# Kernel optimization log

Measured on AMD Instinct MI355X. Metric: run time of the kernel, lower is better.

Reference implementation:

```python
import jax, jax.numpy as jnp
import numpy as np

NV = 1_000_000   # number of 'var' nodes
NC = 500_000     # number of 'con' nodes
E = 16_000_000   # number of v2c edges (c2v is the reverse edge set)
H = 10           # n_h_feats


def setup_inputs() -> dict:
    key = jax.random.key(0)
    ks = jax.random.split(key, 24)
    s = 0.1  # weight init scale
    inp = {
        "var_c": jax.random.normal(ks[0], (NV,), jnp.float32),
        "var_x": jax.random.normal(ks[1], (NV,), jnp.float32),
        "con_b": jax.random.normal(ks[2], (NC,), jnp.float32),
        "A": jax.random.uniform(ks[3], (E,), jnp.float32),
        "src": jax.random.randint(ks[4], (E,), 0, NV, jnp.int32),
        "dst": jax.random.randint(ks[5], (E,), 0, NC, jnp.int32),
        # var_emb / con_emb Linear params
        "Wv": jax.random.normal(ks[6], (2, H), jnp.float32) * s,
        "bv": jnp.zeros((H,), jnp.float32),
        "Wc": jax.random.normal(ks[7], (1, H), jnp.float32) * s,
        "bc": jnp.zeros((H,), jnp.float32),
        # conv1 (GraphConv, shared across v2c/c2v) -- note: its output is
        # overwritten in the original forward and never reaches the output
        "W1": jax.random.normal(ks[8], (H, H), jnp.float32) * s,
        "b1": jnp.zeros((H,), jnp.float32),
        # conv2 (GraphConv, shared across v2c/c2v)
        "W2": jax.random.normal(ks[9], (H, H), jnp.float32) * s,
        "b2": jnp.zeros((H,), jnp.float32),
        # output MLP
        "Wo1": jax.random.normal(ks[10], (H, H), jnp.float32) * s,
        "bo1": jnp.zeros((H,), jnp.float32),
        "Wo2": jax.random.normal(ks[11], (H, H), jnp.float32) * s,
        "bo2": jnp.zeros((H,), jnp.float32),
        "Wo3": jax.random.normal(ks[12], (H, 1), jnp.float32) * s,
        "bo3": jnp.zeros((1,), jnp.float32),
    }
    return inp


def _gconv(x_src, W, b, s_idx, d_idx, ew, norm_src, norm_dst, n_dst):
    # DGL GraphConv, norm='both', with edge weights; in==out feats so W first.
    h = (x_src * norm_src) @ W                      # [N_src, H]
    msg = h[s_idx] * ew[:, None]                    # gather + edge weight
    agg = jax.ops.segment_sum(msg, d_idx, num_segments=n_dst)
    return agg * norm_dst + b


def reference(var_c, var_x, con_b, A, src, dst,
              Wv, bv, Wc, bc, W1, b1, W2, b2,
              Wo1, bo1, Wo2, bo2, Wo3, bo3):
    # symmetric norm from UNWEIGHTED degrees (DGL GraphConv norm='both'),
    # clamped at 1. v2c: out-deg(var), in-deg(con); c2v is the reverse.
    ones_e = jnp.ones_like(A)
    deg_v = jnp.clip(jax.ops.segment_sum(ones_e, src, num_segments=NV), 1.0)
    deg_c = jnp.clip(jax.ops.segment_sum(ones_e, dst, num_segments=NC), 1.0)
    norm_v = deg_v[:, None] ** -0.5
    norm_c = deg_c[:, None] ** -0.5

    # node embeddings
    var_feats = jnp.stack([var_c, var_x], axis=1)   # [NV, 2]
    X_var = jax.nn.relu(var_feats @ Wv + bv)        # [NV, H]
    X_con = jax.nn.relu(con_b[:, None] @ Wc + bc)   # [NC, H] (unused by convs: GraphConv ignores dst feats)

    # In the original forward, conv1 outputs (h_con / h_var) are immediately
    # overwritten by conv2 outputs (GraphConv only consumes src features),
    # so only conv2 lies on the effective compute path.
    h_con = jax.nn.relu(_gconv(X_var, W2, b2, src, dst, A, norm_v, norm_c, NC))
    h_var = jax.nn.relu(_gconv(h_con, W2, b2, dst, src, A, norm_c, norm_v, NV))

    h = jax.nn.relu(h_var @ Wo1 + bo1)
    h = jax.nn.relu(h @ Wo2 + bo2)
    logit = h @ Wo3 + bo3                           # [NV, 1]
    # dgl.readout_nodes(op='mean', ntype='var'), single graph -> [1, 1]
    return jnp.mean(logit, axis=0, keepdims=True)
```

## Files before the change

kernel.cpp:

```cpp
#include <hip/hip_runtime.h>

#define HF 10
#define ST 16
#define BST 16
#define SLC 256
#define NBINS 4096


__global__ __launch_bounds__(1024) void k_hist(const int* __restrict__ idx,
                                               unsigned* __restrict__ hist,
                                               long long s_begin, long long s_end, int per) {
    __shared__ unsigned l[NBINS];
    int t = threadIdx.x, sl = blockIdx.x;
    for (int b = t; b < NBINS; b += 1024) l[b] = 0u;
    __syncthreads();
    long long s0 = s_begin + (long long)sl * per;
    long long s1 = s0 + per; if (s1 > s_end) s1 = s_end;
    for (long long i = s0 + t; i < s1; i += 1024)
        atomicAdd(&l[((unsigned)idx[i]) >> 8], 1u);
    __syncthreads();
    unsigned* out = hist + (size_t)sl * NBINS;
    for (int b = t; b < NBINS; b += 1024) out[b] = l[b];
}

__global__ void k_coltot(const unsigned* __restrict__ h, unsigned* __restrict__ colT) {
    int b = blockIdx.x * 256 + threadIdx.x;
    unsigned s = 0u;
    for (int sl = 0; sl < SLC; sl++) s += h[(size_t)sl * NBINS + b];
    colT[b] = s;
}

__global__ __launch_bounds__(1024) void k_prefix(const unsigned* __restrict__ colT,
                                                 unsigned* __restrict__ start) {
    __shared__ unsigned p[1024];
    int t = threadIdx.x;
    uint4 v = *(const uint4*)(colT + 4 * t);
    unsigned own = v.x + v.y + v.z + v.w;
    p[t] = own;
    __syncthreads();
    for (int off = 1; off < 1024; off <<= 1) {
        unsigned u = (t >= off) ? p[t - off] : 0u;
        __syncthreads();
        p[t] += u;
        __syncthreads();
    }
    unsigned e = p[t] - own;
    *(uint4*)(start + 4 * t) = make_uint4(e, e + v.x, e + v.x + v.y, e + v.x + v.y + v.z);
    if (t == 1023) start[NBINS] = p[1023];
}

__global__ void k_offs(unsigned* __restrict__ h, const unsigned* __restrict__ start) {
    int b = blockIdx.x * 256 + threadIdx.x;
    unsigned cur = start[b];
    for (int sl = 0; sl < SLC; sl++) {
        unsigned* cell = h + (size_t)sl * NBINS + b;
        unsigned v = *cell;
        *cell = cur;
        cur += v;
    }
}

__global__ __launch_bounds__(1024) void k_scatS(const int* __restrict__ src, const int* __restrict__ dst,
                                                const float* __restrict__ A,
                                                const unsigned* __restrict__ offs,
                                                uint2* __restrict__ ebufS,
                                                long long E, int per) {
    __shared__ unsigned cur[NBINS];
    int t = threadIdx.x, sl = blockIdx.x;
    const unsigned* o = offs + (size_t)sl * NBINS;
    for (int b = t; b < NBINS; b += 1024) cur[b] = o[b];
    __syncthreads();
    long long s0 = (long long)sl * per;
    long long s1 = s0 + per; if (s1 > E) s1 = E;
    for (long long i = s0 + t; i < s1; i += 1024) {
        unsigned s = (unsigned)src[i], d = (unsigned)dst[i];
        float a = A[i];
        unsigned pos = atomicAdd(&cur[s >> 8], 1u);
        ebufS[pos] = make_uint2(((s & 255u) << 19) | d, __float_as_uint(a));
    }
}

__global__ void k_cntS2(const uint2* __restrict__ ebufS, const unsigned* __restrict__ startS,
                        const float* __restrict__ var_c, const float* __restrict__ var_x,
                        float4* __restrict__ vcx, int NV) {
    __shared__ unsigned cnt[256];
    int t = threadIdx.x, b = blockIdx.x;
    cnt[t] = 0u;
    __syncthreads();
    unsigned i0 = startS[b], i1 = startS[b + 1];
    for (unsigned i = i0 + t; i < i1; i += 256)
        atomicAdd(&cnt[ebufS[i].x >> 19], 1u);
    __syncthreads();
    int v = b * 256 + t;
    if (v < NV)
        vcx[v] = make_float4(var_c[v], var_x[v], rsqrtf(fmaxf((float)cnt[t], 1.0f)), 0.0f);
}

__global__ __launch_bounds__(1024) void k_scatD(const int* __restrict__ src, const int* __restrict__ dst,
                                                const float* __restrict__ A,
                                                const unsigned* __restrict__ offs,
                                                const float4* __restrict__ vcx,
                                                uint4* __restrict__ ebufD,
                                                long long s_begin, long long s_end, int per) {
    __shared__ unsigned cur[NBINS];
    int t = threadIdx.x, sl = blockIdx.x;
    const unsigned* o = offs + (size_t)sl * NBINS;
    for (int b = t; b < NBINS; b += 1024) cur[b] = o[b];
    __syncthreads();
    long long s0 = s_begin + (long long)sl * per;
    long long s1 = s0 + per; if (s1 > s_end) s1 = s_end;
    for (long long i = s0 + t; i < s1; i += 4096) {
        unsigned sv[4], dv[4]; float av[4]; bool hv[4];
#pragma unroll
        for (int j = 0; j < 4; j++) {
            long long idx = i + (long long)j * 1024;
            hv[j] = idx < s1;
            if (hv[j]) { sv[j] = (unsigned)src[idx]; dv[j] = (unsigned)dst[idx]; av[j] = A[idx]; }
            else       { sv[j] = 0u; dv[j] = 0u; av[j] = 0.0f; }
        }
        float4 g[4];
#pragma unroll
        for (int j = 0; j < 4; j++)
            if (hv[j]) g[j] = vcx[sv[j]];
#pragma unroll
        for (int j = 0; j < 4; j++) {
            if (!hv[j]) continue;
            unsigned pos = atomicAdd(&cur[dv[j] >> 8], 1u);
            ebufD[pos] = make_uint4(dv[j] & 255u, __float_as_uint(av[j] * g[j].z),
                                    __float_as_uint(g[j].x), __float_as_uint(g[j].y));
        }
    }
}

__global__ void k_aggD(const uint4* __restrict__ ebufD, const unsigned* __restrict__ startD,
                       const float* __restrict__ Wv, const float* __restrict__ bv,
                       float* __restrict__ bufC, float* __restrict__ deg_c, int NC) {
    __shared__ float acc[256 * HF];
    __shared__ unsigned cnt[256];
    int t = threadIdx.x, b = blockIdx.x;
    for (int i = t; i < 256 * HF; i += 256) acc[i] = 0.0f;
    cnt[t] = 0u;
    float wv0[HF], wv1[HF], bvv[HF];
#pragma unroll
    for (int h = 0; h < HF; h++) { wv0[h] = Wv[h]; wv1[h] = Wv[HF + h]; bvv[h] = bv[h]; }
    __syncthreads();
    unsigned i0 = startD[b], i1 = startD[b + 1];
    for (unsigned i = i0 + t; i < i1; i += 256) {
        uint4 kv = ebufD[i];
        unsigned dl = kv.x;
        float anv = __uint_as_float(kv.y);
        float c   = __uint_as_float(kv.z);
        float x   = __uint_as_float(kv.w);
        float* ac = acc + dl * HF;
#pragma unroll
        for (int h = 0; h < HF; h++) {
            float e = fmaxf(fmaf(c, wv0[h], fmaf(x, wv1[h], bvv[h])), 0.0f);
            atomicAdd(ac + h, anv * e);
        }
        atomicAdd(&cnt[dl], 1u);
    }
    __syncthreads();
    int gid = b * 256 + t;
    if (gid < NC) {
        float* row = bufC + (size_t)gid * BST;
#pragma unroll
        for (int h = 0; h < HF; h++) row[h] += acc[t * HF + h];
        deg_c[gid] += (float)cnt[t];
    }
}

__global__ void k_conT(float* __restrict__ bufC, const float* __restrict__ deg_c,
                       const float* __restrict__ W2, const float* __restrict__ b2, int NC) {
    __shared__ float sW[HF * HF], sb[HF];
    int t = threadIdx.x;
    if (t < HF * HF) sW[t] = W2[t];
    if (t < HF)      sb[t] = b2[t];
    __syncthreads();
    int i = blockIdx.x * 256 + t;
    if (i >= NC) return;
    float nc = rsqrtf(fmaxf(deg_c[i], 1.0f));
    float* row = bufC + (size_t)i * BST;
    float x[HF];
#pragma unroll
    for (int h = 0; h < HF; h++) x[h] = row[h];
#pragma unroll
    for (int j = 0; j < HF; j++) {
        float a = 0.0f;
#pragma unroll
        for (int k = 0; k < HF; k++) a = fmaf(x[k], sW[k * HF + j], a);
        row[j] = fmaxf(fmaf(a, nc, sb[j]), 0.0f) * nc;
    }
}

__global__ void k_aggS(const uint2* __restrict__ ebufS, const unsigned* __restrict__ startS,
                       const float* __restrict__ bufC, const float4* __restrict__ vcx,
                       const float* __restrict__ W2, const float* __restrict__ b2,
                       const float* __restrict__ Wo1, const float* __restrict__ bo1,
                       const float* __restrict__ Wo2, const float* __restrict__ bo2,
                       const float* __restrict__ Wo3, const float* __restrict__ bo3,
                       double* __restrict__ gacc, int NV) {
    __shared__ float acc[256 * HF];
    __shared__ float sW2[HF * HF], sb2[HF], sW1[HF * HF], sb1[HF], sWm[HF * HF], sbm[HF], sW3[HF];
    __shared__ float sb3;
    __shared__ double red[256];
    int t = threadIdx.x, b = blockIdx.x;
    for (int i = t; i < 256 * HF; i += 256) acc[i] = 0.0f;
    if (t < HF * HF) { sW2[t] = W2[t]; sW1[t] = Wo1[t]; sWm[t] = Wo2[t]; }
    if (t < HF)      { sb2[t] = b2[t]; sb1[t] = bo1[t]; sbm[t] = bo2[t]; sW3[t] = Wo3[t]; }
    if (t == 0)      sb3 = bo3[0];
    __syncthreads();
    unsigned i0 = startS[b], i1 = startS[b + 1];
    int grp = t >> 2;
    int q   = t & 3;
    int nq  = (q < 2) ? 4 : (q == 2 ? 2 : 0);
    for (unsigned base = i0; base < i1; base += 64) {
        unsigned e = base + (unsigned)grp;
        bool ok = e < i1;
        uint2 kv = ok ? ebufS[e] : make_uint2(0u, 0u);
        float4 y = make_float4(0.f, 0.f, 0.f, 0.f);
        if (ok) y = *(const float4*)(bufC + (size_t)(kv.x & 0x7FFFFu) * BST + 4 * q);
        if (ok && nq) {
            float a = __uint_as_float(kv.y);
            float* ac = acc + (kv.x >> 19) * HF + 4 * q;
            atomicAdd(ac + 0, a * y.x);
            atomicAdd(ac + 1, a * y.y);
            if (nq == 4) {
                atomicAdd(ac + 2, a * y.z);
                atomicAdd(ac + 3, a * y.w);
            }
        }
    }
    __syncthreads();
    double local = 0.0;
    int v = b * 256 + t;
    if (v < NV) {
        float nv = vcx[v].z;
        float x[HF], hvv[HF], h1[HF], h2[HF];
#pragma unroll
        for (int h = 0; h < HF; h++) x[h] = acc[t * HF + h];
#pragma unroll
        for (int j = 0; j < HF; j++) {
            float a = 0.0f;
#pragma unroll
            for (int k = 0; k < HF; k++) a = fmaf(x[k], sW2[k * HF + j], a);
            hvv[j] = fmaxf(fmaf(a, nv, sb2[j]), 0.0f);
        }
#pragma unroll
        for (int j = 0; j < HF; j++) {
            float a = sb1[j];
#pragma unroll
            for (int k = 0; k < HF; k++) a = fmaf(hvv[k], sW1[k * HF + j], a);
            h1[j] = fmaxf(a, 0.0f);
        }
#pragma unroll
        for (int j = 0; j < HF; j++) {
            float a = sbm[j];
#pragma unroll
            for (int k = 0; k < HF; k++) a = fmaf(h1[k], sWm[k * HF + j], a);
            h2[j] = fmaxf(a, 0.0f);
        }
        float logit = sb3;
#pragma unroll
        for (int k = 0; k < HF; k++) logit = fmaf(h2[k], sW3[k], logit);
        local = (double)logit;
    }
    red[t] = local;
    __syncthreads();
    for (int s = 128; s > 0; s >>= 1) {
        if (t < s) red[t] += red[t + s];
        __syncthreads();
    }
    if (t == 0) atomicAdd(gacc, red[0]);
}

__global__ void k_out(const double* __restrict__ acc, float* __restrict__ out, int NV) {
    out[0] = (float)(acc[0] / (double)NV);
}


__global__ void k_degree(const int* __restrict__ src, const int* __restrict__ dst,
                         float* __restrict__ deg_v, float* __restrict__ deg_c, int E) {
    int i = blockIdx.x * blockDim.x + threadIdx.x;
    if (i < E) {
        atomicAdd(&deg_v[src[i]], 1.0f);
        atomicAdd(&deg_c[dst[i]], 1.0f);
    }
}

__global__ void k_norm(float* __restrict__ d, int n) {
    int i = blockIdx.x * blockDim.x + threadIdx.x;
    if (i < n) d[i] = 1.0f / sqrtf(fmaxf(d[i], 1.0f));
}

__global__ void k_var_emb(const float* __restrict__ var_c, const float* __restrict__ var_x,
                          const float* __restrict__ norm_v,
                          const float* __restrict__ Wv, const float* __restrict__ bv,
                          const float* __restrict__ W2,
                          float* __restrict__ out, int NV) {
    __shared__ float sWv[2 * HF], sbv[HF], sW2[HF * HF];
    int t = threadIdx.x;
    if (t < 2 * HF) sWv[t] = Wv[t];
    if (t < HF)     sbv[t] = bv[t];
    if (t < HF * HF) sW2[t] = W2[t];
    __syncthreads();
    int i = blockIdx.x * blockDim.x + t;
    if (i >= NV) return;
    float c = var_c[i], x = var_x[i], nv = norm_v[i];
    float e[HF];
#pragma unroll
    for (int h = 0; h < HF; h++)
        e[h] = fmaxf(fmaf(c, sWv[h], fmaf(x, sWv[HF + h], sbv[h])), 0.0f) * nv;
    float* row = out + (size_t)i * ST;
#pragma unroll
    for (int j = 0; j < HF; j++) {
        float acc = 0.0f;
#pragma unroll
        for (int k = 0; k < HF; k++) acc = fmaf(e[k], sW2[k * HF + j], acc);
        row[j] = acc;
    }
}

__global__ void k_edge(const int* __restrict__ gidx, const int* __restrict__ didx,
                       const float* __restrict__ A,
                       const float* __restrict__ h, float* __restrict__ agg, int E) {
    int tid = blockIdx.x * blockDim.x + threadIdx.x;
    int e = tid / 5;
    if (e >= E) return;
    int q = tid - e * 5;
    int s = gidx[e], d = didx[e];
    float a = A[e];
    const float2 m = *(const float2*)(h + (size_t)s * ST + 2 * q);
    float* o = agg + (size_t)d * ST + 2 * q;
    atomicAdd(o,     m.x * a);
    atomicAdd(o + 1, m.y * a);
}

__global__ void k_con(float* __restrict__ buf, const float* __restrict__ norm_c,
                      const float* __restrict__ W2, const float* __restrict__ b2, int NC) {
    __shared__ float sW2[HF * HF], sb2[HF];
    int t = threadIdx.x;
    if (t < HF * HF) sW2[t] = W2[t];
    if (t < HF)      sb2[t] = b2[t];
    __syncthreads();
    int i = blockIdx.x * blockDim.x + t;
    if (i >= NC) return;
    float nc = norm_c[i];
    float* row = buf + (size_t)i * ST;
    float hc[HF];
#pragma unroll
    for (int h = 0; h < HF; h++)
        hc[h] = fmaxf(fmaf(row[h], nc, sb2[h]), 0.0f) * nc;
#pragma unroll
    for (int j = 0; j < HF; j++) {
        float acc = 0.0f;
#pragma unroll
        for (int k = 0; k < HF; k++) acc = fmaf(hc[k], sW2[k * HF + j], acc);
        row[j] = acc;
    }
}

__global__ void k_final(const float* __restrict__ agg_v, const float* __restrict__ norm_v,
                        const float* __restrict__ b2,
                        const float* __restrict__ Wo1, const float* __restrict__ bo1,
                        const float* __restrict__ Wo2, const float* __restrict__ bo2,
                        const float* __restrict__ Wo3, const float* __restrict__ bo3,
                        double* __restrict__ acc, int NV) {
    __shared__ float sb2[HF], sW1[HF * HF], sb1[HF], sW2m[HF * HF], sb2m[HF], sW3[HF];
    __shared__ float sb3;
    __shared__ double red[256];
    int t = threadIdx.x;
    if (t < HF)      sb2[t]  = b2[t];
    if (t < HF * HF) sW1[t]  = Wo1[t];
    if (t < HF)      sb1[t]  = bo1[t];
    if (t < HF * HF) sW2m[t] = Wo2[t];
    if (t < HF)      sb2m[t] = bo2[t];
    if (t < HF)      sW3[t]  = Wo3[t];
    if (t == 0)      sb3     = bo3[0];
    __syncthreads();
    int i = blockIdx.x * blockDim.x + t;
    double local = 0.0;
    if (i < NV) {
        float nv = norm_v[i];
        const float* row = agg_v + (size_t)i * ST;
        float v[HF], h1[HF], h2[HF];
#pragma unroll
        for (int h = 0; h < HF; h++) v[h] = fmaxf(fmaf(row[h], nv, sb2[h]), 0.0f);
#pragma unroll
        for (int j = 0; j < HF; j++) {
            float a = sb1[j];
#pragma unroll
            for (int k = 0; k < HF; k++) a = fmaf(v[k], sW1[k * HF + j], a);
            h1[j] = fmaxf(a, 0.0f);
        }
#pragma unroll
        for (int j = 0; j < HF; j++) {
            float a = sb2m[j];
#pragma unroll
            for (int k = 0; k < HF; k++) a = fmaf(h1[k], sW2m[k * HF + j], a);
            h2[j] = fmaxf(a, 0.0f);
        }
        float logit = sb3;
#pragma unroll
        for (int k = 0; k < HF; k++) logit = fmaf(h2[k], sW3[k], logit);
        local = (double)logit;
    }
    red[t] = local;
    __syncthreads();
    for (int s = 128; s > 0; s >>= 1) {
        if (t < s) red[t] += red[t + s];
        __syncthreads();
    }
    if (t == 0) atomicAdd(acc, red[0]);
}


extern "C" void kernel_launch(void* const* d_in, const int* in_sizes, int n_in,
                              void* d_out, int out_size, void* d_ws, size_t ws_size,
                              hipStream_t stream) {
    const float* var_c = (const float*)d_in[0];
    const float* var_x = (const float*)d_in[1];
    const float* A   = (const float*)d_in[3];
    const int*   src = (const int*)d_in[4];
    const int*   dst = (const int*)d_in[5];
    const float* Wv  = (const float*)d_in[6];
    const float* bv  = (const float*)d_in[7];
    const float* W2  = (const float*)d_in[12];
    const float* b2  = (const float*)d_in[13];
    const float* Wo1 = (const float*)d_in[14];
    const float* bo1 = (const float*)d_in[15];
    const float* Wo2 = (const float*)d_in[16];
    const float* bo2 = (const float*)d_in[17];
    const float* Wo3 = (const float*)d_in[18];
    const float* bo3 = (const float*)d_in[19];

    const int NV = in_sizes[0];
    const int NC = in_sizes[2];
    const int E  = in_sizes[3];

    auto layout_bytes = [&](int nDc, size_t* offs_out) -> size_t {
        size_t off = 0;
        auto alloc = [&](size_t bytes, int slot) {
            if (offs_out) offs_out[slot] = off;
            off = (off + bytes + 255) & ~(size_t)255;
        };
        size_t EcMax = ((size_t)E + nDc - 1) / nDc;
        alloc((size_t)NC * BST * 4, 0);
        alloc((size_t)NV * 16, 1);
        alloc((size_t)NC * 4, 2);
        alloc((size_t)SLC * NBINS * 4, 3);
        alloc((size_t)SLC * NBINS * 4, 4);
        alloc((size_t)NBINS * 4, 5);
        alloc((size_t)(NBINS + 1) * 4, 6);
        alloc((size_t)(NBINS + 1) * 4, 7);
        alloc(8, 8);
        alloc((size_t)E * 8, 9);
        alloc(EcMax * 16, 10);
        return off;
    };

    int nD = 0;
    size_t offs[11];
    for (int cand = 2; cand <= 16; cand++) {
        if (layout_bytes(cand, nullptr) <= ws_size) { nD = cand; break; }
    }
    bool fast = (nD > 0) && (NV <= (1 << 20)) && (NC <= (1 << 19)) && (E > 0);

    char* ws = (char*)d_ws;
    if (fast) {
        layout_bytes(nD, offs);
        float*    bufC   = (float*)(ws + offs[0]);
        float4*   vcx    = (float4*)(ws + offs[1]);
        float*    deg_c  = (float*)(ws + offs[2]);
        unsigned* hS     = (unsigned*)(ws + offs[3]);
        unsigned* hD     = (unsigned*)(ws + offs[4]);
        unsigned* colT   = (unsigned*)(ws + offs[5]);
        unsigned* startS = (unsigned*)(ws + offs[6]);
        unsigned* startD = (unsigned*)(ws + offs[7]);
        double*   gacc   = (double*)(ws + offs[8]);
        uint2*    ebufS  = (uint2*)(ws + offs[9]);
        uint4*    ebufD  = (uint4*)(ws + offs[10]);

        const long long EcMax = ((long long)E + nD - 1) / nD;
        const int perS = (int)(((long long)E + SLC - 1) / SLC);
        const int perD = (int)((EcMax + SLC - 1) / SLC);
        const int NB_S = (NV + 255) >> 8;
        const int NB_C = (NC + 255) >> 8;

        hipMemsetAsync(bufC,  0, (size_t)NC * BST * 4, stream);
        hipMemsetAsync(deg_c, 0, (size_t)NC * 4, stream);
        hipMemsetAsync(gacc,  0, 8, stream);

        k_hist<<<SLC, 1024, 0, stream>>>(src, hS, 0, E, perS);
        k_coltot<<<NBINS / 256, 256, 0, stream>>>(hS, colT);
        k_prefix<<<1, 1024, 0, stream>>>(colT, startS);
        k_offs<<<NBINS / 256, 256, 0, stream>>>(hS, startS);
        k_scatS<<<SLC, 1024, 0, stream>>>(src, dst, A, hS, ebufS, E, perS);

        k_cntS2<<<NB_S, 256, 0, stream>>>(ebufS, startS, var_c, var_x, vcx, NV);

        for (int c = 0; c < nD; c++) {
            long long cb = (long long)c * EcMax;
            long long ce = cb + EcMax; if (ce > E) ce = E;
            k_hist<<<SLC, 1024, 0, stream>>>(dst, hD, cb, ce, perD);
            k_coltot<<<NBINS / 256, 256, 0, stream>>>(hD, colT);
            k_prefix<<<1, 1024, 0, stream>>>(colT, startD);
            k_offs<<<NBINS / 256, 256, 0, stream>>>(hD, startD);
            k_scatD<<<SLC, 1024, 0, stream>>>(src, dst, A, hD, vcx, ebufD, cb, ce, perD);
            k_aggD<<<NB_C, 256, 0, stream>>>(ebufD, startD, Wv, bv, bufC, deg_c, NC);
        }
        k_conT<<<NB_C, 256, 0, stream>>>(bufC, deg_c, W2, b2, NC);

        k_aggS<<<NB_S, 256, 0, stream>>>(ebufS, startS, bufC, vcx, W2, b2,
                                         Wo1, bo1, Wo2, bo2, Wo3, bo3, gacc, NV);
        k_out<<<1, 1, 0, stream>>>(gacc, (float*)d_out, NV);
    } else {
        const int B = 256;
        float* fbufV = (float*)ws;
        float* fbufC = (float*)(ws + (size_t)NV * ST * 4);
        float* deg_v = (float*)(ws + (size_t)(NV + NC) * ST * 4);
        float* deg_c = deg_v + NV;
        size_t acc_off = ((size_t)(NV + NC) * ST * 4 + (size_t)(NV + NC) * 4 + 7) & ~(size_t)7;
        double* acc = (double*)(ws + acc_off);

        hipMemsetAsync(deg_v, 0, (size_t)(NV + NC) * 4, stream);
        hipMemsetAsync(fbufC, 0, (size_t)NC * ST * 4, stream);
        hipMemsetAsync(acc, 0, sizeof(double), stream);

        k_degree<<<(E + B - 1) / B, B, 0, stream>>>(src, dst, deg_v, deg_c, E);
        k_norm<<<(NV + NC + B - 1) / B, B, 0, stream>>>(deg_v, NV + NC);
        k_var_emb<<<(NV + B - 1) / B, B, 0, stream>>>(var_c, var_x, deg_v, Wv, bv, W2, fbufV, NV);

        long long tE = (long long)E * 5;
        k_edge<<<(int)((tE + B - 1) / B), B, 0, stream>>>(src, dst, A, fbufV, fbufC, E);
        k_con<<<(NC + B - 1) / B, B, 0, stream>>>(fbufC, deg_c, W2, b2, NC);

        hipMemsetAsync(fbufV, 0, (size_t)NV * ST * 4, stream);
        k_edge<<<(int)((tE + B - 1) / B), B, 0, stream>>>(dst, src, A, fbufC, fbufV, E);

        k_final<<<(NV + B - 1) / B, B, 0, stream>>>(fbufV, deg_v, b2, Wo1, bo1, Wo2, bo2, Wo3, bo3, acc, NV);
        k_out<<<1, 1, 0, stream>>>(acc, (float*)d_out, NV);
    }
}
```

Before: 3.009 ms.

## Sub-sort src-bucketed edges by dst slice and build dst chunks from them

Adds a second partitioning pass that splits each src bucket into 8 dst-slices (by the high bits of dst), so the edge buffer is ordered by src bin, then dst slice. The dst-side chunked histogram and scatter now read this pre-sorted buffer per src-bin range instead of re-reading the raw src/dst/A arrays. Each chunk then gathers vcx with locality (contiguous var bins) rather than randomly. The cost is two extra full passes over the edge buffer and a scratch buffer sized for the worst-case chunk, which relies on a heuristic bound that could overflow on skewed inputs.

```diff
diff --git a/kernel.cpp b/kernel.cpp
--- a/kernel.cpp
+++ b/kernel.cpp
@@ -5,6 +5,7 @@
 #define BST 16
 #define SLC 256
 #define NBINS 4096
+#define NSL 8
 
 
 __global__ __launch_bounds__(1024) void k_hist(const int* __restrict__ idx,
@@ -80,6 +81,36 @@
     }
 }
 
+__global__ void k_sliceCnt(const uint2* __restrict__ ebufA, const unsigned* __restrict__ startS,
+                           unsigned* __restrict__ startS2) {
+    __shared__ unsigned c8[NSL];
+    int t = threadIdx.x, b = blockIdx.x;
+    if (t < NSL) c8[t] = 0u;
+    __syncthreads();
+    unsigned i0 = startS[b], i1 = startS[b + 1];
+    for (unsigned i = i0 + t; i < i1; i += 256)
+        atomicAdd(&c8[(ebufA[i].x & 0x7FFFFu) >> 16], 1u);
+    __syncthreads();
+    if (t == 0) {
+        unsigned run = i0;
+        for (int s = 0; s < NSL; s++) { startS2[b * NSL + s] = run; run += c8[s]; }
+    }
+}
+
+__global__ void k_sliceScat(const uint2* __restrict__ ebufA, const unsigned* __restrict__ startS,
+                            const unsigned* __restrict__ startS2, uint2* __restrict__ ebufB) {
+    __shared__ unsigned cur[NSL];
+    int t = threadIdx.x, b = blockIdx.x;
+    if (t < NSL) cur[t] = startS2[b * NSL + t];
+    __syncthreads();
+    unsigned i0 = startS[b], i1 = startS[b + 1];
+    for (unsigned i = i0 + t; i < i1; i += 256) {
+        uint2 kv = ebufA[i];
+        unsigned pos = atomicAdd(&cur[(kv.x & 0x7FFFFu) >> 16], 1u);
+        ebufB[pos] = kv;
+    }
+}
+
 __global__ void k_cntS2(const uint2* __restrict__ ebufS, const unsigned* __restrict__ startS,
                         const float* __restrict__ var_c, const float* __restrict__ var_x,
                         float4* __restrict__ vcx, int NV) {
@@ -94,6 +125,48 @@
     int v = b * 256 + t;
     if (v < NV)
         vcx[v] = make_float4(var_c[v], var_x[v], rsqrtf(fmaxf((float)cnt[t], 1.0f)), 0.0f);
+}
+
+__global__ __launch_bounds__(1024) void k_histD2(const uint2* __restrict__ ebufB,
+                                                 const unsigned* __restrict__ startS,
+                                                 unsigned* __restrict__ hist, int B0, int binsPer) {
+    __shared__ unsigned l[NBINS];
+    int t = threadIdx.x, sl = blockIdx.x;
+    for (int b = t; b < NBINS; b += 1024) l[b] = 0u;
+    __syncthreads();
+    int b0 = B0 + sl * binsPer;
+    unsigned i0 = startS[b0], i1 = startS[b0 + binsPer];
+    for (unsigned i = i0 + t; i < i1; i += 1024)
+        atomicAdd(&l[(ebufB[i].x & 0x7FFFFu) >> 8], 1u);
+    __syncthreads();
+    unsigned* out = hist + (size_t)sl * NBINS;
+    for (int b = t; b < NBINS; b += 1024) out[b] = l[b];
+}
+
+__global__ __launch_bounds__(1024) void k_scatD2(const uint2* __restrict__ ebufB,
+                                                 const unsigned* __restrict__ startS,
+                                                 const unsigned* __restrict__ offs,
+                                                 const float4* __restrict__ vcx,
+                                                 uint4* __restrict__ ebufD, int B0, int binsPer) {
+    __shared__ unsigned cur[NBINS];
+    int t = threadIdx.x, sl = blockIdx.x;
+    const unsigned* o = offs + (size_t)sl * NBINS;
+    for (int b = t; b < NBINS; b += 1024) cur[b] = o[b];
+    __syncthreads();
+    int b0 = B0 + sl * binsPer;
+    for (int bb = 0; bb < binsPer; bb++) {
+        int bin = b0 + bb;
+        unsigned vbase = ((unsigned)bin) << 8;
+        unsigned i0 = startS[bin], i1 = startS[bin + 1];
+        for (unsigned i = i0 + t; i < i1; i += 1024) {
+            uint2 kv = ebufB[i];
+            unsigned d = kv.x & 0x7FFFFu;
+            float4 g = vcx[vbase | (kv.x >> 19)];
+            unsigned pos = atomicAdd(&cur[d >> 8], 1u);
+            ebufD[pos] = make_uint4(d & 255u, __float_as_uint(__uint_as_float(kv.y) * g.z),
+                                    __float_as_uint(g.x), __float_as_uint(g.y));
+        }
+    }
 }
 
 __global__ __launch_bounds__(1024) void k_scatD(const int* __restrict__ src, const int* __restrict__ dst,
@@ -437,13 +510,22 @@
     const int NC = in_sizes[2];
     const int E  = in_sizes[3];
 
-    auto layout_bytes = [&](int nDc, size_t* offs_out) -> size_t {
+    auto layout_bytes = [&](int nDc, bool split, size_t* offs_out) -> size_t {
         size_t off = 0;
         auto alloc = [&](size_t bytes, int slot) {
             if (offs_out) offs_out[slot] = off;
             off = (off + bytes + 255) & ~(size_t)255;
         };
-        size_t EcMax = ((size_t)E + nDc - 1) / nDc;
+        size_t EcMax;
+        if (split) {
+            long long vspan = (long long)(NBINS / nDc) * 256;
+            if (vspan > NV) vspan = NV;
+            long long ec = ((long long)E * vspan + NV - 1) / NV + (long long)E / 64;
+            if (ec > E) ec = E;
+            EcMax = (size_t)ec;
+        } else {
+            EcMax = ((size_t)E + nDc - 1) / nDc;
+        }
         alloc((size_t)NC * BST * 4, 0);
         alloc((size_t)NV * 16, 1);
         alloc((size_t)NC * 4, 2);
@@ -454,20 +536,28 @@
         alloc((size_t)(NBINS + 1) * 4, 7);
         alloc(8, 8);
         alloc((size_t)E * 8, 9);
-        alloc(EcMax * 16, 10);
+        size_t scratch = EcMax * 16;
+        if (split && scratch < (size_t)E * 8) scratch = (size_t)E * 8;
+        alloc(scratch, 10);
+        alloc(split ? (size_t)NBINS * NSL * 4 : (size_t)0, 11);
         return off;
     };
 
     int nD = 0;
-    size_t offs[11];
-    for (int cand = 2; cand <= 16; cand++) {
-        if (layout_bytes(cand, nullptr) <= ws_size) { nD = cand; break; }
+    bool split = false;
+    size_t offs[12];
+    for (int cand : {2, 4, 8, 16}) {
+        if (layout_bytes(cand, true, nullptr) <= ws_size) { nD = cand; split = true; break; }
+    }
+    if (nD == 0) {
+        for (int cand = 2; cand <= 16; cand++)
+            if (layout_bytes(cand, false, nullptr) <= ws_size) { nD = cand; break; }
     }
     bool fast = (nD > 0) && (NV <= (1 << 20)) && (NC <= (1 << 19)) && (E > 0);
 
     char* ws = (char*)d_ws;
     if (fast) {
-        layout_bytes(nD, offs);
+        layout_bytes(nD, split, offs);
         float*    bufC   = (float*)(ws + offs[0]);
         float4*   vcx    = (float4*)(ws + offs[1]);
         float*    deg_c  = (float*)(ws + offs[2]);
@@ -477,12 +567,11 @@
         unsigned* startS = (unsigned*)(ws + offs[6]);
         unsigned* startD = (unsigned*)(ws + offs[7]);
         double*   gacc   = (double*)(ws + offs[8]);
-        uint2*    ebufS  = (uint2*)(ws + offs[9]);
-        uint4*    ebufD  = (uint4*)(ws + offs[10]);
-
-        const long long EcMax = ((long long)E + nD - 1) / nD;
+        uint2*    ebufP  = (uint2*)(ws + offs[9]);
+        char*     scr    = ws + offs[10];
+        unsigned* startS2 = (unsigned*)(ws + offs[11]);
+
         const int perS = (int)(((long long)E + SLC - 1) / SLC);
-        const int perD = (int)((EcMax + SLC - 1) / SLC);
         const int NB_S = (NV + 255) >> 8;
         const int NB_C = (NC + 255) >> 8;
 
@@ -490,27 +579,59 @@
         hipMemsetAsync(deg_c, 0, (size_t)NC * 4, stream);
         hipMemsetAsync(gacc,  0, 8, stream);
 
-        k_hist<<<SLC, 1024, 0, stream>>>(src, hS, 0, E, perS);
-        k_coltot<<<NBINS / 256, 256, 0, stream>>>(hS, colT);
-        k_prefix<<<1, 1024, 0, stream>>>(colT, startS);
-        k_offs<<<NBINS / 256, 256, 0, stream>>>(hS, startS);
-        k_scatS<<<SLC, 1024, 0, stream>>>(src, dst, A, hS, ebufS, E, perS);
-
-        k_cntS2<<<NB_S, 256, 0, stream>>>(ebufS, startS, var_c, var_x, vcx, NV);
-
-        for (int c = 0; c < nD; c++) {
-            long long cb = (long long)c * EcMax;
-            long long ce = cb + EcMax; if (ce > E) ce = E;
-            k_hist<<<SLC, 1024, 0, stream>>>(dst, hD, cb, ce, perD);
-            k_coltot<<<NBINS / 256, 256, 0, stream>>>(hD, colT);
-            k_prefix<<<1, 1024, 0, stream>>>(colT, startD);
-            k_offs<<<NBINS / 256, 256, 0, stream>>>(hD, startD);
-            k_scatD<<<SLC, 1024, 0, stream>>>(src, dst, A, hD, vcx, ebufD, cb, ce, perD);
-            k_aggD<<<NB_C, 256, 0, stream>>>(ebufD, startD, Wv, bv, bufC, deg_c, NC);
+        if (split) {
+            uint2* ebufA = (uint2*)scr;
+            uint4* ebufD = (uint4*)scr;
+
+            k_hist<<<SLC, 1024, 0, stream>>>(src, hS, 0, E, perS);
+            k_coltot<<<NBINS / 256, 256, 0, stream>>>(hS, colT);
+            k_prefix<<<1, 1024, 0, stream>>>(colT, startS);
+            k_offs<<<NBINS / 256, 256, 0, stream>>>(hS, startS);
+            k_scatS<<<SLC, 1024, 0, stream>>>(src, dst, A, hS, ebufA, E, perS);
+
+            k_sliceCnt<<<NBINS, 256, 0, stream>>>(ebufA, startS, startS2);
+            k_sliceScat<<<NBINS, 256, 0, stream>>>(ebufA, startS, startS2, ebufP);
+
+            k_cntS2<<<NB_S, 256, 0, stream>>>(ebufP, startS, var_c, var_x, vcx, NV);
+
+            const int binsChunk = NBINS / nD;
+            const int binsPer   = binsChunk / SLC;
+            for (int c = 0; c < nD; c++) {
+                int B0 = c * binsChunk;
+                k_histD2<<<SLC, 1024, 0, stream>>>(ebufP, startS, hD, B0, binsPer);
+                k_coltot<<<NBINS / 256, 256, 0, stream>>>(hD, colT);
+                k_prefix<<<1, 1024, 0, stream>>>(colT, startD);
+                k_offs<<<NBINS / 256, 256, 0, stream>>>(hD, startD);
+                k_scatD2<<<SLC, 1024, 0, stream>>>(ebufP, startS, hD, vcx, ebufD, B0, binsPer);
+                k_aggD<<<NB_C, 256, 0, stream>>>(ebufD, startD, Wv, bv, bufC, deg_c, NC);
+            }
+        } else {
+            uint4* ebufD = (uint4*)scr;
+            const long long EcMax = ((long long)E + nD - 1) / nD;
+            const int perD = (int)((EcMax + SLC - 1) / SLC);
+
+            k_hist<<<SLC, 1024, 0, stream>>>(src, hS, 0, E, perS);
+            k_coltot<<<NBINS / 256, 256, 0, stream>>>(hS, colT);
+            k_prefix<<<1, 1024, 0, stream>>>(colT, startS);
+            k_offs<<<NBINS / 256, 256, 0, stream>>>(hS, startS);
+            k_scatS<<<SLC, 1024, 0, stream>>>(src, dst, A, hS, ebufP, E, perS);
+
+            k_cntS2<<<NB_S, 256, 0, stream>>>(ebufP, startS, var_c, var_x, vcx, NV);
+
+            for (int c = 0; c < nD; c++) {
+                long long cb = (long long)c * EcMax;
+                long long ce = cb + EcMax; if (ce > E) ce = E;
+                k_hist<<<SLC, 1024, 0, stream>>>(dst, hD, cb, ce, perD);
+                k_coltot<<<NBINS / 256, 256, 0, stream>>>(hD, colT);
+                k_prefix<<<1, 1024, 0, stream>>>(colT, startD);
+                k_offs<<<NBINS / 256, 256, 0, stream>>>(hD, startD);
+                k_scatD<<<SLC, 1024, 0, stream>>>(src, dst, A, hD, vcx, ebufD, cb, ce, perD);
+                k_aggD<<<NB_C, 256, 0, stream>>>(ebufD, startD, Wv, bv, bufC, deg_c, NC);
+            }
         }
         k_conT<<<NB_C, 256, 0, stream>>>(bufC, deg_c, W2, b2, NC);
 
-        k_aggS<<<NB_S, 256, 0, stream>>>(ebufS, startS, bufC, vcx, W2, b2,
+        k_aggS<<<NB_S, 256, 0, stream>>>(ebufP, startS, bufC, vcx, W2, b2,
                                          Wo1, bo1, Wo2, bo2, Wo3, bo3, gacc, NV);
         k_out<<<1, 1, 0, stream>>>(gacc, (float*)d_out, NV);
     } else {
```

New measurement: 2.997 ms. About the same (-0.4%).
